# Optimization experiments

Hardware: AMD Instinct MI355X
Metric: run time of the kernel (lower is better)

## Reference

```python
import jax, jax.numpy as jnp
import numpy as np

B, S, E, H, FF = 4, 2048, 512, 8, 2048
DH = E // H
EPS = 1e-6


def setup_inputs() -> dict:
    key = jax.random.key(0)
    ks = jax.random.split(key, 16)
    sc = lambda fan_in: 1.0 / np.sqrt(fan_in)
    inp = {
        "x": jax.random.normal(ks[0], (B, S, E), dtype=jnp.float32),
        "src_mask": jnp.ones((B, 1, 1, S), dtype=jnp.int32),
        # attention projections, stored [in, out]
        "wq": jax.random.uniform(ks[1], (E, E), minval=-sc(E), maxval=sc(E)),
        "bq": jnp.zeros((E,), jnp.float32),
        "wk": jax.random.uniform(ks[2], (E, E), minval=-sc(E), maxval=sc(E)),
        "bk": jnp.zeros((E,), jnp.float32),
        "wv": jax.random.uniform(ks[3], (E, E), minval=-sc(E), maxval=sc(E)),
        "bv": jnp.zeros((E,), jnp.float32),
        "wo": jax.random.uniform(ks[4], (E, E), minval=-sc(E), maxval=sc(E)),
        "bo": jnp.zeros((E,), jnp.float32),
        # feed-forward
        "w1": jax.random.uniform(ks[5], (E, FF), minval=-sc(E), maxval=sc(E)),
        "b1": jnp.zeros((FF,), jnp.float32),
        "w2": jax.random.uniform(ks[6], (FF, E), minval=-sc(FF), maxval=sc(FF)),
        "b2": jnp.zeros((E,), jnp.float32),
        # addNormLayer scalar params (alpha init 1, bias init 0)
        "alpha1": jnp.ones((1,), jnp.float32),
        "beta1": jnp.zeros((1,), jnp.float32),
        "alpha2": jnp.ones((1,), jnp.float32),
        "beta2": jnp.zeros((1,), jnp.float32),
    }
    return inp


def _norm(x, alpha, beta):
    # matches torch: mean + unbiased std (ddof=1), eps added to std
    mean = jnp.mean(x, axis=-1, keepdims=True)
    std = jnp.std(x, axis=-1, keepdims=True, ddof=1)
    return alpha * (x - mean) / (std + EPS) + beta


def reference(x, src_mask, wq, bq, wk, bk, wv, bv, wo, bo,
              w1, b1, w2, b2, alpha1, beta1, alpha2, beta2):
    # --- residual 1: pre-norm self-attention ---
    n = _norm(x, alpha1, beta1)  # [B,S,E]
    q = (n @ wq + bq).reshape(B, S, H, DH).transpose(0, 2, 1, 3)  # [B,H,S,DH]
    k = (n @ wk + bk).reshape(B, S, H, DH).transpose(0, 2, 1, 3)
    v = (n @ wv + bv).reshape(B, S, H, DH).transpose(0, 2, 1, 3)
    scores = jnp.einsum('bhqd,bhkd->bhqk', q, k) / np.sqrt(DH)  # [B,H,S,S]
    scores = jnp.where(src_mask == 0, -1e9, scores)
    attn = jax.nn.softmax(scores, axis=-1)
    ctx = jnp.einsum('bhqk,bhkd->bhqd', attn, v)  # [B,H,S,DH]
    ctx = ctx.transpose(0, 2, 1, 3).reshape(B, S, E)
    x = x + (ctx @ wo + bo)
    # --- residual 2: pre-norm FFN ---
    n2 = _norm(x, alpha2, beta2)
    ff = jax.nn.relu(n2 @ w1 + b1) @ w2 + b2
    return x + ff
```

## Files before the change

### kernel.cpp

```cpp
#include <hip/hip_runtime.h>

typedef __bf16 bfrag __attribute__((ext_vector_type(8)));
typedef float f32x4 __attribute__((ext_vector_type(4)));
typedef unsigned short us8 __attribute__((ext_vector_type(8)));

__device__ __forceinline__ float bf2f(unsigned short s) {
  unsigned u = ((unsigned)s) << 16;
  float f;
  __builtin_memcpy(&f, &u, 4);
  return f;
}
__device__ __forceinline__ unsigned short f2bf(float f) {
  unsigned u;
  __builtin_memcpy(&u, &f, 4);
  u += 0x7fffu + ((u >> 16) & 1u);
  return (unsigned short)(u >> 16);
}
__device__ __forceinline__ float rdf(const void* p, size_t i, int isf) {
  return isf ? ((const float*)p)[i] : bf2f(((const unsigned short*)p)[i]);
}
__device__ __forceinline__ void gld16(const unsigned short* g, unsigned short* l) {
  __builtin_amdgcn_global_load_lds(
      (const __attribute__((address_space(1))) unsigned int*)g,
      (__attribute__((address_space(3))) unsigned int*)l, 16, 0, 0);
}

__global__ __launch_bounds__(256) void detect_k(
    const unsigned short* __restrict__ x, int* __restrict__ flag) {
  __shared__ int cnt;
  if (threadIdx.x == 0) cnt = 0;
  __syncthreads();
  int c = 0;
  for (int i = threadIdx.x; i < 4096; i += 256) {
    unsigned short s = x[2 * i];
    int e = (s >> 7) & 0xFF;
    if (e > 0xC2 || (e != 0 && e < 0x3D)) c++;
  }
  atomicAdd(&cnt, c);
  __syncthreads();
  if (threadIdx.x == 0) flag[0] = (cnt > 256) ? 1 : 0;
}

__global__ __launch_bounds__(256) void prep_k(
    const void* wq, const void* wk, const void* wv, const void* wo,
    const void* w1, const void* w2,
    unsigned short* wqT, unsigned short* wkT, unsigned short* wvT,
    unsigned short* woT, unsigned short* w1T, unsigned short* w2T,
    const void* bq, const void* bk, const void* bv, const void* bo,
    const void* b1, const void* b2, float* __restrict__ bcat,
    const int* __restrict__ flag) {
  __shared__ unsigned short tile[32][33];
  int isf = flag[0];
  int bid = blockIdx.x;
  int tid = threadIdx.x;
  if (bid >= 3072) {
    int i = (bid - 3072) * 256 + tid;
    if (i >= 4608) return;
    float v;
    if (i < 512) v = rdf(bq, i, isf);
    else if (i < 1024) v = rdf(bk, i - 512, isf);
    else if (i < 1536) v = rdf(bv, i - 1024, isf);
    else if (i < 2048) v = rdf(bo, i - 1536, isf);
    else if (i < 4096) v = rdf(b1, i - 2048, isf);
    else v = rdf(b2, i - 4096, isf);
    bcat[i] = v;
    return;
  }
  const void* W;
  unsigned short* Wt;
  int K, N, t;
  if (bid < 1024) {
    K = 512; N = 512; t = bid & 255;
    if (bid < 256) { W = wq; Wt = wqT; }
    else if (bid < 512) { W = wk; Wt = wkT; }
    else if (bid < 768) { W = wv; Wt = wvT; }
    else { W = wo; Wt = woT; }
  } else if (bid < 2048) {
    W = w1; Wt = w1T; K = 512; N = 2048; t = bid - 1024;
  } else {
    W = w2; Wt = w2T; K = 2048; N = 512; t = bid - 2048;
  }
  int nx = N >> 5;
  int n0 = (t % nx) * 32, k0 = (t / nx) * 32;
#pragma unroll
  for (int i = 0; i < 4; i++) {
    int e = tid + i * 256;
    int r = e >> 5, c = e & 31;
    tile[r][c] = f2bf(rdf(W, (size_t)(k0 + r) * N + n0 + c, isf));
  }
  __syncthreads();
#pragma unroll
  for (int i = 0; i < 4; i++) {
    int e = tid + i * 256;
    int r = e >> 5, c = e & 31;
    Wt[(size_t)(n0 + r) * K + k0 + c] = tile[c][r];
  }
}

__global__ __launch_bounds__(256) void vtrans_k(
    const unsigned short* __restrict__ qkb, unsigned short* __restrict__ vbt) {
  __shared__ unsigned short tile[32][33];
  int tid = threadIdx.x;
  int s0 = blockIdx.x * 32;
  int d0 = blockIdx.y * 32;
  int bh = blockIdx.z, b = bh >> 3, h = bh & 7;
#pragma unroll
  for (int i = 0; i < 4; i++) {
    int e = tid + i * 256;
    int r = e >> 5, c = e & 31;
    tile[r][c] = qkb[((size_t)b * 2048 + s0 + r) * 1536 + 1024 + h * 64 + d0 + c];
  }
  __syncthreads();
#pragma unroll
  for (int i = 0; i < 4; i++) {
    int e = tid + i * 256;
    int r = e >> 5, c = e & 31;
    vbt[((size_t)bh * 64 + d0 + r) * 2048 + s0 + c] = tile[c][r];
  }
}

template <int XMODE>
__global__ __launch_bounds__(256) void norm_k(
    const void* __restrict__ xin, const void* __restrict__ alpha,
    const void* __restrict__ beta, unsigned short* __restrict__ out,
    const int* __restrict__ flag) {
  constexpr int E = 512;
  int isf = flag[0];
  int xf = XMODE ? 1 : isf;
  int tid = threadIdx.x;
  int wave = tid >> 6, lane = tid & 63;
  size_t tok = (size_t)blockIdx.x * 4 + wave;
  float v[8];
  if (xf) {
    const float* xp = (const float*)xin + tok * E + lane * 8;
    float4 a0 = *(const float4*)xp;
    float4 a1 = *(const float4*)(xp + 4);
    v[0] = a0.x; v[1] = a0.y; v[2] = a0.z; v[3] = a0.w;
    v[4] = a1.x; v[5] = a1.y; v[6] = a1.z; v[7] = a1.w;
  } else {
    us8 u = *(const us8*)((const unsigned short*)xin + tok * E + lane * 8);
#pragma unroll
    for (int j = 0; j < 8; j++) v[j] = bf2f(u[j]);
  }
  float s = 0.f, sq = 0.f;
#pragma unroll
  for (int j = 0; j < 8; j++) { s += v[j]; sq += v[j] * v[j]; }
#pragma unroll
  for (int off = 1; off < 64; off <<= 1) {
    s += __shfl_xor(s, off, 64);
    sq += __shfl_xor(sq, off, 64);
  }
  float mean = s * (1.0f / 512.0f);
  float var = fmaxf((sq - 512.0f * mean * mean) * (1.0f / 511.0f), 0.0f);
  float inv = rdf(alpha, 0, isf) / (sqrtf(var) + 1e-6f);
  float be = rdf(beta, 0, isf);
  us8 ov;
#pragma unroll
  for (int j = 0; j < 8; j++) ov[j] = f2bf((v[j] - mean) * inv + be);
  *(us8*)((unsigned short*)out + tok * E + lane * 8) = ov;
}

template <int TN, int RES, int OUTM, int RELU>
__global__ __launch_bounds__(256) void gemm2_k(
    const unsigned short* __restrict__ A,
    const unsigned short* __restrict__ Bt,
    const float* __restrict__ bias,
    const void* __restrict__ res,
    void* __restrict__ outp,
    int N, int K, const int* __restrict__ flag) {
  constexpr int MT = (TN == 128) ? 4 : 2;
  __shared__ alignas(16) unsigned short As[128 * 32];
  __shared__ alignas(16) unsigned short Bs[TN * 32];
  int isf = flag[0];
  int outf32 = (OUTM == 1) || (OUTM == 2 && isf);
  int tid = threadIdx.x;
  int wave = tid >> 6, lane = tid & 63;
  int quad = lane >> 4, l16 = lane & 15;
  int wm = (TN == 128) ? (wave >> 1) : wave;
  int wn = (TN == 128) ? (wave & 1) : 0;
  size_t m0 = (size_t)blockIdx.x * 128;
  size_t n0 = (size_t)blockIdx.y * TN;

  int lrow = lane >> 2;
  int kseg = (lane & 3) * 8;

  const unsigned short* ag = A + (m0 + wave * 16 + lrow) * K + kseg;
  const unsigned short* bg = Bt + (n0 + wave * 16 + lrow) * K + kseg;
  unsigned short* asl = &As[(wave * 16) * 32];
  unsigned short* bsl = &Bs[(wave * 16) * 32];

  f32x4 acc[MT][4];
#pragma unroll
  for (int i = 0; i < MT; i++)
#pragma unroll
    for (int j = 0; j < 4; j++) acc[i][j] = {0.f, 0.f, 0.f, 0.f};

  for (int k0 = 0; k0 < K; k0 += 32) {
    __syncthreads();
    gld16(ag + k0, asl);
    gld16(ag + (size_t)64 * K + k0, asl + 64 * 32);
    gld16(bg + k0, bsl);
    if (TN == 128) gld16(bg + (size_t)64 * K + k0, bsl + 64 * 32);
    __syncthreads();
    bfrag af[MT], bf[4];
#pragma unroll
    for (int i = 0; i < MT; i++)
      af[i] = *(const bfrag*)&As[(wm * (MT * 16) + i * 16 + l16) * 32 + quad * 8];
#pragma unroll
    for (int j = 0; j < 4; j++)
      bf[j] = *(const bfrag*)&Bs[(wn * 64 + j * 16 + l16) * 32 + quad * 8];
#pragma unroll
    for (int i = 0; i < MT; i++)
#pragma unroll
      for (int j = 0; j < 4; j++)
        acc[i][j] = __builtin_amdgcn_mfma_f32_16x16x32_bf16(af[i], bf[j], acc[i][j], 0, 0, 0);
  }
#pragma unroll
  for (int j = 0; j < 4; j++) {
    size_t n = n0 + wn * 64 + j * 16 + l16;
    float bv = bias[n];
#pragma unroll
    for (int i = 0; i < MT; i++) {
#pragma unroll
      for (int r = 0; r < 4; r++) {
        size_t m = m0 + wm * (MT * 16) + i * 16 + quad * 4 + r;
        float vv = acc[i][j][r] + bv;
        if (RELU) vv = fmaxf(vv, 0.0f);
        if (RES == 1) vv += rdf(res, m * N + n, isf);
        else if (RES == 2) vv += ((const float*)res)[m * N + n];
        if (outf32) ((float*)outp)[m * N + n] = vv;
        else ((unsigned short*)outp)[m * N + n] = f2bf(vv);
      }
    }
  }
}

__global__ __launch_bounds__(256) void attn_k(
    const unsigned short* __restrict__ qkb,
    const unsigned short* __restrict__ vbt,
    const int* __restrict__ mask,
    unsigned short* __restrict__ ctx) {
  constexpr int S = 2048;
  __shared__ alignas(16) unsigned short Kt[64][72];
  __shared__ alignas(16) unsigned short Vt[64][72];
  __shared__ alignas(16) unsigned short Pl[4][16][68];
  __shared__ float mskf[64];
  int tid = threadIdx.x, wave = tid >> 6, lane = tid & 63;
  int quad = lane >> 4, l16 = lane & 15;
  int q0 = blockIdx.x * 64;
  int bh = blockIdx.y, b = bh >> 3, h = bh & 7;
  size_t rowbase = (size_t)b * S;

  bfrag qf0, qf1;
  {
    const unsigned short* qp =
        qkb + (rowbase + q0 + wave * 16 + l16) * 1536 + h * 64 + quad * 8;
    qf0 = *(const bfrag*)qp;
    qf1 = *(const bfrag*)(qp + 32);
  }
  f32x4 o[4] = {{0, 0, 0, 0}, {0, 0, 0, 0}, {0, 0, 0, 0}, {0, 0, 0, 0}};
  float l_i[4] = {0.f, 0.f, 0.f, 0.f};

  int srow = tid >> 2;
  int c0 = (tid & 3) * 8;
  const unsigned short* kbase = qkb + 512 + h * 64;
  const unsigned short* vrow = vbt + ((size_t)bh * 64 + srow) * S;
  const float SC = 0.18033688f;

  for (int kt = 0; kt < S; kt += 64) {
    __syncthreads();
    {
      const unsigned short* kp = kbase + (rowbase + kt + srow) * 1536;
      *(uint4*)&Kt[srow][c0]      = *(const uint4*)(kp + c0);
      *(uint4*)&Kt[srow][c0 + 32] = *(const uint4*)(kp + c0 + 32);
      *(uint4*)&Vt[srow][c0]      = *(const uint4*)(vrow + kt + c0);
      *(uint4*)&Vt[srow][c0 + 32] = *(const uint4*)(vrow + kt + c0 + 32);
    }
    if (tid < 64) mskf[tid] = mask[rowbase + kt + tid] ? 0.0f : -1e5f;
    __syncthreads();

    float pr[4][4];
#pragma unroll
    for (int nt = 0; nt < 4; nt++) {
      f32x4 s = {0, 0, 0, 0};
      bfrag k0f = *(const bfrag*)&Kt[nt * 16 + l16][quad * 8];
      bfrag k1f = *(const bfrag*)&Kt[nt * 16 + l16][32 + quad * 8];
      s = __builtin_amdgcn_mfma_f32_16x16x32_bf16(qf0, k0f, s, 0, 0, 0);
      s = __builtin_amdgcn_mfma_f32_16x16x32_bf16(qf1, k1f, s, 0, 0, 0);
      float mb = mskf[nt * 16 + l16];
#pragma unroll
      for (int r = 0; r < 4; r++) {
        float p = __builtin_amdgcn_exp2f(fminf(fmaf(s[r], SC, mb), 50.0f));
        pr[nt][r] = p;
        unsigned u;
        __builtin_memcpy(&u, &p, 4);
        Pl[wave][quad * 4 + r][nt * 16 + l16] = (unsigned short)(u >> 16);
      }
    }
#pragma unroll
    for (int r = 0; r < 4; r++)
      l_i[r] += (pr[0][r] + pr[1][r]) + (pr[2][r] + pr[3][r]);
    bfrag pa0 = *(const bfrag*)&Pl[wave][l16][quad * 8];
    bfrag pa1 = *(const bfrag*)&Pl[wave][l16][32 + quad * 8];
#pragma unroll
    for (int dt = 0; dt < 4; dt++) {
      bfrag v0 = *(const bfrag*)&Vt[dt * 16 + l16][quad * 8];
      bfrag v1 = *(const bfrag*)&Vt[dt * 16 + l16][32 + quad * 8];
      o[dt] = __builtin_amdgcn_mfma_f32_16x16x32_bf16(pa0, v0, o[dt], 0, 0, 0);
      o[dt] = __builtin_amdgcn_mfma_f32_16x16x32_bf16(pa1, v1, o[dt], 0, 0, 0);
    }
  }
#pragma unroll
  for (int r = 0; r < 4; r++) {
#pragma unroll
    for (int off = 1; off < 16; off <<= 1) l_i[r] += __shfl_xor(l_i[r], off, 64);
    l_i[r] = 1.0f / fmaxf(l_i[r], 1e-30f);
  }
#pragma unroll
  for (int dt = 0; dt < 4; dt++) {
#pragma unroll
    for (int r = 0; r < 4; r++) {
      size_t qrow = rowbase + q0 + wave * 16 + quad * 4 + r;
      ctx[qrow * 512 + h * 64 + dt * 16 + l16] = f2bf(o[dt][r] * l_i[r]);
    }
  }
}

extern "C" void kernel_launch(void* const* d_in, const int* in_sizes, int n_in,
                              void* d_out, int out_size, void* d_ws, size_t ws_size,
                              hipStream_t stream) {
  const unsigned short* x = (const unsigned short*)d_in[0];
  const int* mask         = (const int*)d_in[1];
  const void* wq = d_in[2];  const void* bq = d_in[3];
  const void* wk = d_in[4];  const void* bk = d_in[5];
  const void* wv = d_in[6];  const void* bv = d_in[7];
  const void* wo = d_in[8];  const void* bo = d_in[9];
  const void* w1 = d_in[10]; const void* b1 = d_in[11];
  const void* w2 = d_in[12]; const void* b2 = d_in[13];
  const void* alpha1 = d_in[14]; const void* beta1 = d_in[15];
  const void* alpha2 = d_in[16]; const void* beta2 = d_in[17];

  char* ws = (char*)d_ws;
  int* flag            = (int*)(ws + 0);
  unsigned short* wqkvT= (unsigned short*)(ws + 65536);
  unsigned short* wqT  = wqkvT;
  unsigned short* wkT  = (unsigned short*)(ws + 589824);
  unsigned short* wvT  = (unsigned short*)(ws + 1114112);
  unsigned short* woT  = (unsigned short*)(ws + 1638400);
  unsigned short* w1T  = (unsigned short*)(ws + 2162688);
  unsigned short* w2T  = (unsigned short*)(ws + 4259840);
  float*          bcat = (float*)         (ws + 6356992);
  float*          x1   = (float*)         (ws + 6422528);
  unsigned short* n1   = (unsigned short*)(ws + 23199744);
  unsigned short* ctx  = n1;
  unsigned short* n2   = n1;
  unsigned short* qkb  = (unsigned short*)(ws + 31588352);
  unsigned short* vbt  = (unsigned short*)(ws + 56754176);
  unsigned short* ff1  = qkb;

  dim3 blk(256);

  detect_k<<<1, blk, 0, stream>>>(x, flag);
  prep_k<<<3090, blk, 0, stream>>>(wq, wk, wv, wo, w1, w2,
                                   wqT, wkT, wvT, woT, w1T, w2T,
                                   bq, bk, bv, bo, b1, b2, bcat, flag);

  norm_k<0><<<2048, blk, 0, stream>>>(x, alpha1, beta1, n1, flag);
  gemm2_k<128, 0, 0, 0><<<dim3(64, 12), blk, 0, stream>>>(n1, wqkvT, bcat, nullptr, qkb, 1536, 512, flag);
  vtrans_k<<<dim3(64, 2, 32), blk, 0, stream>>>(qkb, vbt);
  attn_k<<<dim3(32, 32), blk, 0, stream>>>(qkb, vbt, mask, ctx);
  gemm2_k<64, 1, 1, 0><<<dim3(64, 8), blk, 0, stream>>>(ctx, woT, bcat + 1536, (const void*)x, x1, 512, 512, flag);
  norm_k<1><<<2048, blk, 0, stream>>>(x1, alpha2, beta2, n2, flag);
  gemm2_k<128, 0, 0, 1><<<dim3(64, 16), blk, 0, stream>>>(n2, w1T, bcat + 2048, nullptr, ff1, 2048, 512, flag);
  gemm2_k<64, 2, 2, 0><<<dim3(64, 8), blk, 0, stream>>>(ff1, w2T, bcat + 4096, x1, d_out, 512, 2048, flag);
}
```

Baseline: 324.5 us.

## Merge setup kernels and process two query tiles per attention block

```diff
diff --git a/kernel.cpp b/kernel.cpp
--- a/kernel.cpp
+++ b/kernel.cpp
@@ -25,111 +25,14 @@
       (__attribute__((address_space(3))) unsigned int*)l, 16, 0, 0);
 }
 
-__global__ __launch_bounds__(256) void detect_k(
-    const unsigned short* __restrict__ x, int* __restrict__ flag) {
-  __shared__ int cnt;
-  if (threadIdx.x == 0) cnt = 0;
-  __syncthreads();
-  int c = 0;
-  for (int i = threadIdx.x; i < 4096; i += 256) {
-    unsigned short s = x[2 * i];
-    int e = (s >> 7) & 0xFF;
-    if (e > 0xC2 || (e != 0 && e < 0x3D)) c++;
-  }
-  atomicAdd(&cnt, c);
-  __syncthreads();
-  if (threadIdx.x == 0) flag[0] = (cnt > 256) ? 1 : 0;
-}
-
-__global__ __launch_bounds__(256) void prep_k(
-    const void* wq, const void* wk, const void* wv, const void* wo,
-    const void* w1, const void* w2,
-    unsigned short* wqT, unsigned short* wkT, unsigned short* wvT,
-    unsigned short* woT, unsigned short* w1T, unsigned short* w2T,
-    const void* bq, const void* bk, const void* bv, const void* bo,
-    const void* b1, const void* b2, float* __restrict__ bcat,
-    const int* __restrict__ flag) {
-  __shared__ unsigned short tile[32][33];
-  int isf = flag[0];
-  int bid = blockIdx.x;
-  int tid = threadIdx.x;
-  if (bid >= 3072) {
-    int i = (bid - 3072) * 256 + tid;
-    if (i >= 4608) return;
-    float v;
-    if (i < 512) v = rdf(bq, i, isf);
-    else if (i < 1024) v = rdf(bk, i - 512, isf);
-    else if (i < 1536) v = rdf(bv, i - 1024, isf);
-    else if (i < 2048) v = rdf(bo, i - 1536, isf);
-    else if (i < 4096) v = rdf(b1, i - 2048, isf);
-    else v = rdf(b2, i - 4096, isf);
-    bcat[i] = v;
-    return;
-  }
-  const void* W;
-  unsigned short* Wt;
-  int K, N, t;
-  if (bid < 1024) {
-    K = 512; N = 512; t = bid & 255;
-    if (bid < 256) { W = wq; Wt = wqT; }
-    else if (bid < 512) { W = wk; Wt = wkT; }
-    else if (bid < 768) { W = wv; Wt = wvT; }
-    else { W = wo; Wt = woT; }
-  } else if (bid < 2048) {
-    W = w1; Wt = w1T; K = 512; N = 2048; t = bid - 1024;
-  } else {
-    W = w2; Wt = w2T; K = 2048; N = 512; t = bid - 2048;
-  }
-  int nx = N >> 5;
-  int n0 = (t % nx) * 32, k0 = (t / nx) * 32;
-#pragma unroll
-  for (int i = 0; i < 4; i++) {
-    int e = tid + i * 256;
-    int r = e >> 5, c = e & 31;
-    tile[r][c] = f2bf(rdf(W, (size_t)(k0 + r) * N + n0 + c, isf));
-  }
-  __syncthreads();
-#pragma unroll
-  for (int i = 0; i < 4; i++) {
-    int e = tid + i * 256;
-    int r = e >> 5, c = e & 31;
-    Wt[(size_t)(n0 + r) * K + k0 + c] = tile[c][r];
-  }
-}
-
-__global__ __launch_bounds__(256) void vtrans_k(
-    const unsigned short* __restrict__ qkb, unsigned short* __restrict__ vbt) {
-  __shared__ unsigned short tile[32][33];
-  int tid = threadIdx.x;
-  int s0 = blockIdx.x * 32;
-  int d0 = blockIdx.y * 32;
-  int bh = blockIdx.z, b = bh >> 3, h = bh & 7;
-#pragma unroll
-  for (int i = 0; i < 4; i++) {
-    int e = tid + i * 256;
-    int r = e >> 5, c = e & 31;
-    tile[r][c] = qkb[((size_t)b * 2048 + s0 + r) * 1536 + 1024 + h * 64 + d0 + c];
-  }
-  __syncthreads();
-#pragma unroll
-  for (int i = 0; i < 4; i++) {
-    int e = tid + i * 256;
-    int r = e >> 5, c = e & 31;
-    vbt[((size_t)bh * 64 + d0 + r) * 2048 + s0 + c] = tile[c][r];
-  }
-}
-
 template <int XMODE>
-__global__ __launch_bounds__(256) void norm_k(
-    const void* __restrict__ xin, const void* __restrict__ alpha,
-    const void* __restrict__ beta, unsigned short* __restrict__ out,
-    const int* __restrict__ flag) {
+__device__ void norm_unit(const void* xin, const void* alpha, const void* beta,
+                          unsigned short* out, int isf, int u) {
   constexpr int E = 512;
-  int isf = flag[0];
   int xf = XMODE ? 1 : isf;
   int tid = threadIdx.x;
   int wave = tid >> 6, lane = tid & 63;
-  size_t tok = (size_t)blockIdx.x * 4 + wave;
+  size_t tok = (size_t)u * 4 + wave;
   float v[8];
   if (xf) {
     const float* xp = (const float*)xin + tok * E + lane * 8;
@@ -138,9 +41,9 @@
     v[0] = a0.x; v[1] = a0.y; v[2] = a0.z; v[3] = a0.w;
     v[4] = a1.x; v[5] = a1.y; v[6] = a1.z; v[7] = a1.w;
   } else {
-    us8 u = *(const us8*)((const unsigned short*)xin + tok * E + lane * 8);
-#pragma unroll
-    for (int j = 0; j < 8; j++) v[j] = bf2f(u[j]);
+    us8 uu = *(const us8*)((const unsigned short*)xin + tok * E + lane * 8);
+#pragma unroll
+    for (int j = 0; j < 8; j++) v[j] = bf2f(uu[j]);
   }
   float s = 0.f, sq = 0.f;
 #pragma unroll
@@ -157,7 +60,115 @@
   us8 ov;
 #pragma unroll
   for (int j = 0; j < 8; j++) ov[j] = f2bf((v[j] - mean) * inv + be);
-  *(us8*)((unsigned short*)out + tok * E + lane * 8) = ov;
+  *(us8*)(out + tok * E + lane * 8) = ov;
+}
+
+__global__ __launch_bounds__(256) void setup_k(
+    const unsigned short* __restrict__ x16,
+    const void* wq, const void* wk, const void* wv, const void* wo,
+    const void* w1, const void* w2,
+    unsigned short* wqkvT, unsigned short* woT,
+    unsigned short* w1T, unsigned short* w2T,
+    const void* bq, const void* bk, const void* bv, const void* bo,
+    const void* b1, const void* b2, float* __restrict__ bcat,
+    const void* alpha1, const void* beta1, unsigned short* __restrict__ n1,
+    int* __restrict__ flag) {
+  __shared__ unsigned short tile[32][33];
+  __shared__ int s_cnt;
+  int tid = threadIdx.x;
+  int bid = blockIdx.x;
+  if (tid == 0) s_cnt = 0;
+  __syncthreads();
+  {
+    int c = 0;
+    for (int i = tid; i < 4096; i += 256) {
+      unsigned short s = x16[2 * i];
+      int e = (s >> 7) & 0xFF;
+      if (e > 0xC2 || (e != 0 && e < 0x3D)) c++;
+    }
+    atomicAdd(&s_cnt, c);
+  }
+  __syncthreads();
+  const int isf = (s_cnt > 256) ? 1 : 0;
+  if (bid == 0 && tid == 0) flag[0] = isf;
+
+  if (bid >= 3090) {
+    norm_unit<0>(x16, alpha1, beta1, n1, isf, bid - 3090);
+    return;
+  }
+  if (bid >= 3072) {
+    int i = (bid - 3072) * 256 + tid;
+    if (i < 4608) {
+      float v;
+      if (i < 512) v = rdf(bq, i, isf);
+      else if (i < 1024) v = rdf(bk, i - 512, isf);
+      else if (i < 1536) v = rdf(bv, i - 1024, isf);
+      else if (i < 2048) v = rdf(bo, i - 1536, isf);
+      else if (i < 4096) v = rdf(b1, i - 2048, isf);
+      else v = rdf(b2, i - 4096, isf);
+      bcat[i] = v;
+    }
+    return;
+  }
+  const void* W;
+  unsigned short* Wt;
+  int K, N, t;
+  if (bid < 1024) {
+    K = 512; N = 512; t = bid & 255;
+    if (bid < 256) { W = wq; Wt = wqkvT; }
+    else if (bid < 512) { W = wk; Wt = wqkvT + 262144; }
+    else if (bid < 768) { W = wv; Wt = wqkvT + 524288; }
+    else { W = wo; Wt = woT; }
+  } else if (bid < 2048) {
+    W = w1; Wt = w1T; K = 512; N = 2048; t = bid - 1024;
+  } else {
+    W = w2; Wt = w2T; K = 2048; N = 512; t = bid - 2048;
+  }
+  int nx = N >> 5;
+  int n0 = (t % nx) * 32, k0 = (t / nx) * 32;
+#pragma unroll
+  for (int i = 0; i < 4; i++) {
+    int e = tid + i * 256;
+    int r = e >> 5, c = e & 31;
+    tile[r][c] = f2bf(rdf(W, (size_t)(k0 + r) * N + n0 + c, isf));
+  }
+  __syncthreads();
+#pragma unroll
+  for (int i = 0; i < 4; i++) {
+    int e = tid + i * 256;
+    int r = e >> 5, c = e & 31;
+    Wt[(size_t)(n0 + r) * K + k0 + c] = tile[c][r];
+  }
+}
+
+__global__ __launch_bounds__(256) void vtrans_k(
+    const unsigned short* __restrict__ qkb, unsigned short* __restrict__ vbt) {
+  __shared__ unsigned short tile[32][33];
+  int tid = threadIdx.x;
+  int u = blockIdx.x;
+  int s0 = (u & 63) * 32;
+  int d0 = ((u >> 6) & 1) * 32;
+  int bh = u >> 7, b = bh >> 3, h = bh & 7;
+#pragma unroll
+  for (int i = 0; i < 4; i++) {
+    int e = tid + i * 256;
+    int r = e >> 5, c = e & 31;
+    tile[r][c] = qkb[((size_t)b * 2048 + s0 + r) * 1536 + 1024 + h * 64 + d0 + c];
+  }
+  __syncthreads();
+#pragma unroll
+  for (int i = 0; i < 4; i++) {
+    int e = tid + i * 256;
+    int r = e >> 5, c = e & 31;
+    vbt[((size_t)bh * 64 + d0 + r) * 2048 + s0 + c] = tile[c][r];
+  }
+}
+
+__global__ __launch_bounds__(256) void norm2_k(
+    const void* __restrict__ xin, const void* __restrict__ alpha,
+    const void* __restrict__ beta, unsigned short* __restrict__ out,
+    const int* __restrict__ flag) {
+  norm_unit<1>(xin, alpha, beta, out, flag[0], blockIdx.x);
 }
 
 template <int TN, int RES, int OUTM, int RELU>
@@ -241,25 +252,31 @@
     const int* __restrict__ mask,
     unsigned short* __restrict__ ctx) {
   constexpr int S = 2048;
-  __shared__ alignas(16) unsigned short Kt[64][72];
-  __shared__ alignas(16) unsigned short Vt[64][72];
-  __shared__ alignas(16) unsigned short Pl[4][16][68];
+  __shared__ alignas(16) unsigned short Kt[64][70];
+  __shared__ alignas(16) unsigned short Vt[64][70];
+  __shared__ alignas(16) unsigned short Pl[4][16][70];
   __shared__ float mskf[64];
   int tid = threadIdx.x, wave = tid >> 6, lane = tid & 63;
   int quad = lane >> 4, l16 = lane & 15;
-  int q0 = blockIdx.x * 64;
-  int bh = blockIdx.y, b = bh >> 3, h = bh & 7;
+  int q0 = (blockIdx.x & 15) * 128;
+  int bh = blockIdx.x >> 4, b = bh >> 3, h = bh & 7;
   size_t rowbase = (size_t)b * S;
-
-  bfrag qf0, qf1;
-  {
+  unsigned short* PlW = &Pl[wave][0][0];
+
+  bfrag qf[2][2];
+#pragma unroll
+  for (int mi = 0; mi < 2; mi++) {
     const unsigned short* qp =
-        qkb + (rowbase + q0 + wave * 16 + l16) * 1536 + h * 64 + quad * 8;
-    qf0 = *(const bfrag*)qp;
-    qf1 = *(const bfrag*)(qp + 32);
-  }
-  f32x4 o[4] = {{0, 0, 0, 0}, {0, 0, 0, 0}, {0, 0, 0, 0}, {0, 0, 0, 0}};
-  float l_i[4] = {0.f, 0.f, 0.f, 0.f};
+        qkb + (rowbase + q0 + mi * 64 + wave * 16 + l16) * 1536 + h * 64 + quad * 8;
+    qf[mi][0] = *(const bfrag*)qp;
+    qf[mi][1] = *(const bfrag*)(qp + 32);
+  }
+  f32x4 o[2][4];
+  float l_i[2][4];
+#pragma unroll
+  for (int mi = 0; mi < 2; mi++)
+#pragma unroll
+    for (int j = 0; j < 4; j++) { o[mi][j] = {0.f, 0.f, 0.f, 0.f}; l_i[mi][j] = 0.f; }
 
   int srow = tid >> 2;
   int c0 = (tid & 3) * 8;
@@ -279,49 +296,56 @@
     if (tid < 64) mskf[tid] = mask[rowbase + kt + tid] ? 0.0f : -1e5f;
     __syncthreads();
 
-    float pr[4][4];
-#pragma unroll
-    for (int nt = 0; nt < 4; nt++) {
-      f32x4 s = {0, 0, 0, 0};
-      bfrag k0f = *(const bfrag*)&Kt[nt * 16 + l16][quad * 8];
-      bfrag k1f = *(const bfrag*)&Kt[nt * 16 + l16][32 + quad * 8];
-      s = __builtin_amdgcn_mfma_f32_16x16x32_bf16(qf0, k0f, s, 0, 0, 0);
-      s = __builtin_amdgcn_mfma_f32_16x16x32_bf16(qf1, k1f, s, 0, 0, 0);
-      float mb = mskf[nt * 16 + l16];
+#pragma unroll
+    for (int mi = 0; mi < 2; mi++) {
+      float pr[4][4];
+#pragma unroll
+      for (int nt = 0; nt < 4; nt++) {
+        f32x4 s = {0, 0, 0, 0};
+        bfrag k0f = *(const bfrag*)&Kt[nt * 16 + l16][quad * 8];
+        bfrag k1f = *(const bfrag*)&Kt[nt * 16 + l16][32 + quad * 8];
+        s = __builtin_amdgcn_mfma_f32_16x16x32_bf16(qf[mi][0], k0f, s, 0, 0, 0);
+        s = __builtin_amdgcn_mfma_f32_16x16x32_bf16(qf[mi][1], k1f, s, 0, 0, 0);
+        float mb = mskf[nt * 16 + l16];
+#pragma unroll
+        for (int r = 0; r < 4; r++) {
+          float p = __builtin_amdgcn_exp2f(fminf(fmaf(s[r], SC, mb), 50.0f));
+          pr[nt][r] = p;
+          unsigned u;
+          __builtin_memcpy(&u, &p, 4);
+          PlW[(quad * 4 + r) * 70 + nt * 16 + l16] = (unsigned short)(u >> 16);
+        }
+      }
+#pragma unroll
+      for (int r = 0; r < 4; r++)
+        l_i[mi][r] += (pr[0][r] + pr[1][r]) + (pr[2][r] + pr[3][r]);
+      bfrag pa0 = *(const bfrag*)&PlW[l16 * 70 + quad * 8];
+      bfrag pa1 = *(const bfrag*)&PlW[l16 * 70 + 32 + quad * 8];
+#pragma unroll
+      for (int dt = 0; dt < 4; dt++) {
+        bfrag v0 = *(const bfrag*)&Vt[dt * 16 + l16][quad * 8];
+        bfrag v1 = *(const bfrag*)&Vt[dt * 16 + l16][32 + quad * 8];
+        o[mi][dt] = __builtin_amdgcn_mfma_f32_16x16x32_bf16(pa0, v0, o[mi][dt], 0, 0, 0);
+        o[mi][dt] = __builtin_amdgcn_mfma_f32_16x16x32_bf16(pa1, v1, o[mi][dt], 0, 0, 0);
+      }
+    }
+  }
+#pragma unroll
+  for (int mi = 0; mi < 2; mi++) {
+#pragma unroll
+    for (int r = 0; r < 4; r++) {
+#pragma unroll
+      for (int off = 1; off < 16; off <<= 1)
+        l_i[mi][r] += __shfl_xor(l_i[mi][r], off, 64);
+      l_i[mi][r] = 1.0f / fmaxf(l_i[mi][r], 1e-30f);
+    }
+#pragma unroll
+    for (int dt = 0; dt < 4; dt++) {
 #pragma unroll
       for (int r = 0; r < 4; r++) {
-        float p = __builtin_amdgcn_exp2f(fminf(fmaf(s[r], SC, mb), 50.0f));
-        pr[nt][r] = p;
-        unsigned u;
-        __builtin_memcpy(&u, &p, 4);
-        Pl[wave][quad * 4 + r][nt * 16 + l16] = (unsigned short)(u >> 16);
+        size_t qrow = rowbase + q0 + mi * 64 + wave * 16 + quad * 4 + r;
+        ctx[qrow * 512 + h * 64 + dt * 16 + l16] = f2bf(o[mi][dt][r] * l_i[mi][r]);
       }
-    }
-#pragma unroll
-    for (int r = 0; r < 4; r++)
-      l_i[r] += (pr[0][r] + pr[1][r]) + (pr[2][r] + pr[3][r]);
-    bfrag pa0 = *(const bfrag*)&Pl[wave][l16][quad * 8];
-    bfrag pa1 = *(const bfrag*)&Pl[wave][l16][32 + quad * 8];
-#pragma unroll
-    for (int dt = 0; dt < 4; dt++) {
-      bfrag v0 = *(const bfrag*)&Vt[dt * 16 + l16][quad * 8];
-      bfrag v1 = *(const bfrag*)&Vt[dt * 16 + l16][32 + quad * 8];
-      o[dt] = __builtin_amdgcn_mfma_f32_16x16x32_bf16(pa0, v0, o[dt], 0, 0, 0);
-      o[dt] = __builtin_amdgcn_mfma_f32_16x16x32_bf16(pa1, v1, o[dt], 0, 0, 0);
-    }
-  }
-#pragma unroll
-  for (int r = 0; r < 4; r++) {
-#pragma unroll
-    for (int off = 1; off < 16; off <<= 1) l_i[r] += __shfl_xor(l_i[r], off, 64);
-    l_i[r] = 1.0f / fmaxf(l_i[r], 1e-30f);
-  }
-#pragma unroll
-  for (int dt = 0; dt < 4; dt++) {
-#pragma unroll
-    for (int r = 0; r < 4; r++) {
-      size_t qrow = rowbase + q0 + wave * 16 + quad * 4 + r;
-      ctx[qrow * 512 + h * 64 + dt * 16 + l16] = f2bf(o[dt][r] * l_i[r]);
     }
   }
 }
@@ -343,34 +367,27 @@
   char* ws = (char*)d_ws;
   int* flag            = (int*)(ws + 0);
   unsigned short* wqkvT= (unsigned short*)(ws + 65536);
-  unsigned short* wqT  = wqkvT;
-  unsigned short* wkT  = (unsigned short*)(ws + 589824);
-  unsigned short* wvT  = (unsigned short*)(ws + 1114112);
   unsigned short* woT  = (unsigned short*)(ws + 1638400);
   unsigned short* w1T  = (unsigned short*)(ws + 2162688);
   unsigned short* w2T  = (unsigned short*)(ws + 4259840);
   float*          bcat = (float*)         (ws + 6356992);
   float*          x1   = (float*)         (ws + 6422528);
   unsigned short* n1   = (unsigned short*)(ws + 23199744);
-  unsigned short* ctx  = n1;
-  unsigned short* n2   = n1;
   unsigned short* qkb  = (unsigned short*)(ws + 31588352);
   unsigned short* vbt  = (unsigned short*)(ws + 56754176);
   unsigned short* ff1  = qkb;
 
   dim3 blk(256);
 
-  detect_k<<<1, blk, 0, stream>>>(x, flag);
-  prep_k<<<3090, blk, 0, stream>>>(wq, wk, wv, wo, w1, w2,
-                                   wqT, wkT, wvT, woT, w1T, w2T,
-                                   bq, bk, bv, bo, b1, b2, bcat, flag);
-
-  norm_k<0><<<2048, blk, 0, stream>>>(x, alpha1, beta1, n1, flag);
+  setup_k<<<5138, blk, 0, stream>>>(x, wq, wk, wv, wo, w1, w2,
+                                    wqkvT, woT, w1T, w2T,
+                                    bq, bk, bv, bo, b1, b2, bcat,
+                                    alpha1, beta1, n1, flag);
   gemm2_k<128, 0, 0, 0><<<dim3(64, 12), blk, 0, stream>>>(n1, wqkvT, bcat, nullptr, qkb, 1536, 512, flag);
-  vtrans_k<<<dim3(64, 2, 32), blk, 0, stream>>>(qkb, vbt);
-  attn_k<<<dim3(32, 32), blk, 0, stream>>>(qkb, vbt, mask, ctx);
-  gemm2_k<64, 1, 1, 0><<<dim3(64, 8), blk, 0, stream>>>(ctx, woT, bcat + 1536, (const void*)x, x1, 512, 512, flag);
-  norm_k<1><<<2048, blk, 0, stream>>>(x1, alpha2, beta2, n2, flag);
-  gemm2_k<128, 0, 0, 1><<<dim3(64, 16), blk, 0, stream>>>(n2, w1T, bcat + 2048, nullptr, ff1, 2048, 512, flag);
+  vtrans_k<<<4096, blk, 0, stream>>>(qkb, vbt);
+  attn_k<<<512, blk, 0, stream>>>(qkb, vbt, mask, n1);
+  gemm2_k<64, 1, 1, 0><<<dim3(64, 8), blk, 0, stream>>>(n1, woT, bcat + 1536, (const void*)x, x1, 512, 512, flag);
+  norm2_k<<<2048, blk, 0, stream>>>(x1, alpha2, beta2, n1, flag);
+  gemm2_k<128, 0, 0, 1><<<dim3(64, 16), blk, 0, stream>>>(n1, w1T, bcat + 2048, nullptr, ff1, 2048, 512, flag);
   gemm2_k<64, 2, 2, 0><<<dim3(64, 8), blk, 0, stream>>>(ff1, w2T, bcat + 4096, x1, d_out, 512, 2048, flag);
 }
```

New measurement: 375.7 us. 1.16x slower.

## Fuse all stages into one persistent kernel with software grid barriers

Applied to the files above, without the earlier changes.

```diff
diff --git a/kernel.cpp b/kernel.cpp
--- a/kernel.cpp
+++ b/kernel.cpp
@@ -25,63 +25,51 @@
       (__attribute__((address_space(3))) unsigned int*)l, 16, 0, 0);
 }
 
-__global__ __launch_bounds__(256) void detect_k(
-    const unsigned short* __restrict__ x, int* __restrict__ flag) {
-  __shared__ int cnt;
-  if (threadIdx.x == 0) cnt = 0;
-  __syncthreads();
-  int c = 0;
-  for (int i = threadIdx.x; i < 4096; i += 256) {
-    unsigned short s = x[2 * i];
-    int e = (s >> 7) & 0xFF;
-    if (e > 0xC2 || (e != 0 && e < 0x3D)) c++;
-  }
-  atomicAdd(&cnt, c);
-  __syncthreads();
-  if (threadIdx.x == 0) flag[0] = (cnt > 256) ? 1 : 0;
-}
-
-__global__ __launch_bounds__(256) void prep_k(
-    const void* wq, const void* wk, const void* wv, const void* wo,
-    const void* w1, const void* w2,
-    unsigned short* wqT, unsigned short* wkT, unsigned short* wvT,
-    unsigned short* woT, unsigned short* w1T, unsigned short* w2T,
-    const void* bq, const void* bk, const void* bv, const void* bo,
-    const void* b1, const void* b2, float* __restrict__ bcat,
-    const int* __restrict__ flag) {
-  __shared__ unsigned short tile[32][33];
-  int isf = flag[0];
-  int bid = blockIdx.x;
+struct MArgs {
+  const unsigned short* x16;
+  const int* mask;
+  const void *wq, *wk, *wv, *wo, *w1, *w2;
+  const void *bq, *bk, *bv, *bo, *b1, *b2;
+  const void *alpha1, *beta1, *alpha2, *beta2;
+  void* d_out;
+  unsigned* bar;
+  unsigned* gen;
+  unsigned short* wqkvT;
+  unsigned short* woT;
+  unsigned short* w1T;
+  unsigned short* w2T;
+  float* bcat;
+  float* x1;
+  unsigned short* n1;
+  unsigned short* qkb;
+  unsigned short* vbt;
+};
+
+__device__ __forceinline__ void gbar(unsigned* bar, unsigned* gen, unsigned nb) {
+  __syncthreads();
+  if (threadIdx.x == 0) {
+    __threadfence();
+    unsigned g = __hip_atomic_load(gen, __ATOMIC_RELAXED, __HIP_MEMORY_SCOPE_AGENT);
+    if (atomicAdd(bar, 1u) == nb - 1u) {
+      __hip_atomic_store(bar, 0u, __ATOMIC_RELAXED, __HIP_MEMORY_SCOPE_AGENT);
+      __threadfence();
+      atomicAdd(gen, 1u);
+    } else {
+      while (__hip_atomic_load(gen, __ATOMIC_RELAXED, __HIP_MEMORY_SCOPE_AGENT) == g)
+        __builtin_amdgcn_s_sleep(8);
+      __threadfence();
+    }
+  }
+  __syncthreads();
+}
+
+__device__ void trans_unit(const void* W, unsigned short* Wt, int K, int N,
+                           int t, int isf, char* SM) {
+  auto tile = (unsigned short(*)[33])SM;
   int tid = threadIdx.x;
-  if (bid >= 3072) {
-    int i = (bid - 3072) * 256 + tid;
-    if (i >= 4608) return;
-    float v;
-    if (i < 512) v = rdf(bq, i, isf);
-    else if (i < 1024) v = rdf(bk, i - 512, isf);
-    else if (i < 1536) v = rdf(bv, i - 1024, isf);
-    else if (i < 2048) v = rdf(bo, i - 1536, isf);
-    else if (i < 4096) v = rdf(b1, i - 2048, isf);
-    else v = rdf(b2, i - 4096, isf);
-    bcat[i] = v;
-    return;
-  }
-  const void* W;
-  unsigned short* Wt;
-  int K, N, t;
-  if (bid < 1024) {
-    K = 512; N = 512; t = bid & 255;
-    if (bid < 256) { W = wq; Wt = wqT; }
-    else if (bid < 512) { W = wk; Wt = wkT; }
-    else if (bid < 768) { W = wv; Wt = wvT; }
-    else { W = wo; Wt = woT; }
-  } else if (bid < 2048) {
-    W = w1; Wt = w1T; K = 512; N = 2048; t = bid - 1024;
-  } else {
-    W = w2; Wt = w2T; K = 2048; N = 512; t = bid - 2048;
-  }
   int nx = N >> 5;
   int n0 = (t % nx) * 32, k0 = (t / nx) * 32;
+  __syncthreads();
 #pragma unroll
   for (int i = 0; i < 4; i++) {
     int e = tid + i * 256;
@@ -97,13 +85,14 @@
   }
 }
 
-__global__ __launch_bounds__(256) void vtrans_k(
-    const unsigned short* __restrict__ qkb, unsigned short* __restrict__ vbt) {
-  __shared__ unsigned short tile[32][33];
+__device__ void vtrans_unit(const unsigned short* qkb, unsigned short* vbt,
+                            int u, char* SM) {
+  auto tile = (unsigned short(*)[33])SM;
   int tid = threadIdx.x;
-  int s0 = blockIdx.x * 32;
-  int d0 = blockIdx.y * 32;
-  int bh = blockIdx.z, b = bh >> 3, h = bh & 7;
+  int s0 = (u & 63) * 32;
+  int d0 = ((u >> 6) & 1) * 32;
+  int bh = u >> 7, b = bh >> 3, h = bh & 7;
+  __syncthreads();
 #pragma unroll
   for (int i = 0; i < 4; i++) {
     int e = tid + i * 256;
@@ -120,16 +109,13 @@
 }
 
 template <int XMODE>
-__global__ __launch_bounds__(256) void norm_k(
-    const void* __restrict__ xin, const void* __restrict__ alpha,
-    const void* __restrict__ beta, unsigned short* __restrict__ out,
-    const int* __restrict__ flag) {
+__device__ void norm_unit(const void* xin, const void* alpha, const void* beta,
+                          unsigned short* out, int isf, int u) {
   constexpr int E = 512;
-  int isf = flag[0];
   int xf = XMODE ? 1 : isf;
   int tid = threadIdx.x;
   int wave = tid >> 6, lane = tid & 63;
-  size_t tok = (size_t)blockIdx.x * 4 + wave;
+  size_t tok = (size_t)u * 4 + wave;
   float v[8];
   if (xf) {
     const float* xp = (const float*)xin + tok * E + lane * 8;
@@ -138,9 +124,9 @@
     v[0] = a0.x; v[1] = a0.y; v[2] = a0.z; v[3] = a0.w;
     v[4] = a1.x; v[5] = a1.y; v[6] = a1.z; v[7] = a1.w;
   } else {
-    us8 u = *(const us8*)((const unsigned short*)xin + tok * E + lane * 8);
-#pragma unroll
-    for (int j = 0; j < 8; j++) v[j] = bf2f(u[j]);
+    us8 uu = *(const us8*)((const unsigned short*)xin + tok * E + lane * 8);
+#pragma unroll
+    for (int j = 0; j < 8; j++) v[j] = bf2f(uu[j]);
   }
   float s = 0.f, sq = 0.f;
 #pragma unroll
@@ -157,29 +143,26 @@
   us8 ov;
 #pragma unroll
   for (int j = 0; j < 8; j++) ov[j] = f2bf((v[j] - mean) * inv + be);
-  *(us8*)((unsigned short*)out + tok * E + lane * 8) = ov;
+  *(us8*)(out + tok * E + lane * 8) = ov;
 }
 
 template <int TN, int RES, int OUTM, int RELU>
-__global__ __launch_bounds__(256) void gemm2_k(
-    const unsigned short* __restrict__ A,
-    const unsigned short* __restrict__ Bt,
-    const float* __restrict__ bias,
-    const void* __restrict__ res,
-    void* __restrict__ outp,
-    int N, int K, const int* __restrict__ flag) {
+__device__ void gemm_tile(const unsigned short* __restrict__ A,
+                          const unsigned short* __restrict__ Bt,
+                          const float* __restrict__ bias,
+                          const void* __restrict__ res, void* __restrict__ outp,
+                          int N, int K, int isf, int mi, int ni, char* SM) {
   constexpr int MT = (TN == 128) ? 4 : 2;
-  __shared__ alignas(16) unsigned short As[128 * 32];
-  __shared__ alignas(16) unsigned short Bs[TN * 32];
-  int isf = flag[0];
+  unsigned short* As = (unsigned short*)SM;
+  unsigned short* Bs = (unsigned short*)(SM + 8192);
   int outf32 = (OUTM == 1) || (OUTM == 2 && isf);
   int tid = threadIdx.x;
   int wave = tid >> 6, lane = tid & 63;
   int quad = lane >> 4, l16 = lane & 15;
   int wm = (TN == 128) ? (wave >> 1) : wave;
   int wn = (TN == 128) ? (wave & 1) : 0;
-  size_t m0 = (size_t)blockIdx.x * 128;
-  size_t n0 = (size_t)blockIdx.y * TN;
+  size_t m0 = (size_t)mi * 128;
+  size_t n0 = (size_t)ni * TN;
 
   int lrow = lane >> 2;
   int kseg = (lane & 3) * 8;
@@ -235,20 +218,19 @@
   }
 }
 
-__global__ __launch_bounds__(256) void attn_k(
-    const unsigned short* __restrict__ qkb,
-    const unsigned short* __restrict__ vbt,
-    const int* __restrict__ mask,
-    unsigned short* __restrict__ ctx) {
+__device__ void attn_tile(const unsigned short* __restrict__ qkb,
+                          const unsigned short* __restrict__ vbt,
+                          const int* __restrict__ mask,
+                          unsigned short* __restrict__ ctx,
+                          int q0, int bh, char* SM) {
   constexpr int S = 2048;
-  __shared__ alignas(16) unsigned short Kt[64][72];
-  __shared__ alignas(16) unsigned short Vt[64][72];
-  __shared__ alignas(16) unsigned short Pl[4][16][68];
-  __shared__ float mskf[64];
+  auto Kt = (unsigned short(*)[72])(SM);
+  auto Vt = (unsigned short(*)[72])(SM + 9216);
+  float* mskf = (float*)(SM + 27136);
   int tid = threadIdx.x, wave = tid >> 6, lane = tid & 63;
   int quad = lane >> 4, l16 = lane & 15;
-  int q0 = blockIdx.x * 64;
-  int bh = blockIdx.y, b = bh >> 3, h = bh & 7;
+  unsigned short* PlW = (unsigned short*)(SM + 18432) + wave * 16 * 68;
+  int b = bh >> 3, h = bh & 7;
   size_t rowbase = (size_t)b * S;
 
   bfrag qf0, qf1;
@@ -294,14 +276,14 @@
         pr[nt][r] = p;
         unsigned u;
         __builtin_memcpy(&u, &p, 4);
-        Pl[wave][quad * 4 + r][nt * 16 + l16] = (unsigned short)(u >> 16);
+        PlW[(quad * 4 + r) * 68 + nt * 16 + l16] = (unsigned short)(u >> 16);
       }
     }
 #pragma unroll
     for (int r = 0; r < 4; r++)
       l_i[r] += (pr[0][r] + pr[1][r]) + (pr[2][r] + pr[3][r]);
-    bfrag pa0 = *(const bfrag*)&Pl[wave][l16][quad * 8];
-    bfrag pa1 = *(const bfrag*)&Pl[wave][l16][32 + quad * 8];
+    bfrag pa0 = *(const bfrag*)&PlW[l16 * 68 + quad * 8];
+    bfrag pa1 = *(const bfrag*)&PlW[l16 * 68 + 32 + quad * 8];
 #pragma unroll
     for (int dt = 0; dt < 4; dt++) {
       bfrag v0 = *(const bfrag*)&Vt[dt * 16 + l16][quad * 8];
@@ -326,51 +308,102 @@
   }
 }
 
+__global__ __launch_bounds__(256, 2) void mega_k(MArgs a) {
+  __shared__ alignas(16) char SM[28672];
+  __shared__ int s_cnt;
+  int tid = threadIdx.x;
+  int bid = blockIdx.x;
+
+  if (tid == 0) s_cnt = 0;
+  __syncthreads();
+  {
+    int c = 0;
+    for (int i = tid; i < 4096; i += 256) {
+      unsigned short s = a.x16[2 * i];
+      int e = (s >> 7) & 0xFF;
+      if (e > 0xC2 || (e != 0 && e < 0x3D)) c++;
+    }
+    atomicAdd(&s_cnt, c);
+  }
+  __syncthreads();
+  const int isf = (s_cnt > 256) ? 1 : 0;
+
+  for (int u = bid; u < 5138; u += 512) {
+    if (u < 3072) {
+      if (u < 256)       trans_unit(a.wq, a.wqkvT,          512, 512, u, isf, SM);
+      else if (u < 512)  trans_unit(a.wk, a.wqkvT + 262144, 512, 512, u - 256, isf, SM);
+      else if (u < 768)  trans_unit(a.wv, a.wqkvT + 524288, 512, 512, u - 512, isf, SM);
+      else if (u < 1024) trans_unit(a.wo, a.woT,            512, 512, u - 768, isf, SM);
+      else if (u < 2048) trans_unit(a.w1, a.w1T,  512, 2048, u - 1024, isf, SM);
+      else               trans_unit(a.w2, a.w2T, 2048,  512, u - 2048, isf, SM);
+    } else if (u < 3090) {
+      int i = (u - 3072) * 256 + tid;
+      if (i < 4608) {
+        float v;
+        if (i < 512) v = rdf(a.bq, i, isf);
+        else if (i < 1024) v = rdf(a.bk, i - 512, isf);
+        else if (i < 1536) v = rdf(a.bv, i - 1024, isf);
+        else if (i < 2048) v = rdf(a.bo, i - 1536, isf);
+        else if (i < 4096) v = rdf(a.b1, i - 2048, isf);
+        else v = rdf(a.b2, i - 4096, isf);
+        a.bcat[i] = v;
+      }
+    } else {
+      norm_unit<0>(a.x16, a.alpha1, a.beta1, a.n1, isf, u - 3090);
+    }
+  }
+  gbar(a.bar, a.gen, 512);
+  for (int t = bid; t < 768; t += 512)
+    gemm_tile<128, 0, 0, 0>(a.n1, a.wqkvT, a.bcat, nullptr, a.qkb,
+                            1536, 512, isf, t & 63, t >> 6, SM);
+  gbar(a.bar, a.gen, 512);
+  for (int u = bid; u < 4096; u += 512) vtrans_unit(a.qkb, a.vbt, u, SM);
+  gbar(a.bar, a.gen, 512);
+  for (int t = bid; t < 1024; t += 512)
+    attn_tile(a.qkb, a.vbt, a.mask, a.n1, (t & 31) * 64, t >> 5, SM);
+  gbar(a.bar, a.gen, 512);
+  gemm_tile<64, 1, 1, 0>(a.n1, a.woT, a.bcat + 1536, (const void*)a.x16, a.x1,
+                         512, 512, isf, bid & 63, bid >> 6, SM);
+  gbar(a.bar, a.gen, 512);
+  for (int u = bid; u < 2048; u += 512)
+    norm_unit<1>(a.x1, a.alpha2, a.beta2, a.n1, isf, u);
+  gbar(a.bar, a.gen, 512);
+  for (int t = bid; t < 1024; t += 512)
+    gemm_tile<128, 0, 0, 1>(a.n1, a.w1T, a.bcat + 2048, nullptr, a.qkb,
+                            2048, 512, isf, t & 63, t >> 6, SM);
+  gbar(a.bar, a.gen, 512);
+  gemm_tile<64, 2, 2, 0>(a.qkb, a.w2T, a.bcat + 4096, a.x1, a.d_out,
+                         512, 2048, isf, bid & 63, bid >> 6, SM);
+}
+
 extern "C" void kernel_launch(void* const* d_in, const int* in_sizes, int n_in,
                               void* d_out, int out_size, void* d_ws, size_t ws_size,
                               hipStream_t stream) {
-  const unsigned short* x = (const unsigned short*)d_in[0];
-  const int* mask         = (const int*)d_in[1];
-  const void* wq = d_in[2];  const void* bq = d_in[3];
-  const void* wk = d_in[4];  const void* bk = d_in[5];
-  const void* wv = d_in[6];  const void* bv = d_in[7];
-  const void* wo = d_in[8];  const void* bo = d_in[9];
-  const void* w1 = d_in[10]; const void* b1 = d_in[11];
-  const void* w2 = d_in[12]; const void* b2 = d_in[13];
-  const void* alpha1 = d_in[14]; const void* beta1 = d_in[15];
-  const void* alpha2 = d_in[16]; const void* beta2 = d_in[17];
-
   char* ws = (char*)d_ws;
-  int* flag            = (int*)(ws + 0);
-  unsigned short* wqkvT= (unsigned short*)(ws + 65536);
-  unsigned short* wqT  = wqkvT;
-  unsigned short* wkT  = (unsigned short*)(ws + 589824);
-  unsigned short* wvT  = (unsigned short*)(ws + 1114112);
-  unsigned short* woT  = (unsigned short*)(ws + 1638400);
-  unsigned short* w1T  = (unsigned short*)(ws + 2162688);
-  unsigned short* w2T  = (unsigned short*)(ws + 4259840);
-  float*          bcat = (float*)         (ws + 6356992);
-  float*          x1   = (float*)         (ws + 6422528);
-  unsigned short* n1   = (unsigned short*)(ws + 23199744);
-  unsigned short* ctx  = n1;
-  unsigned short* n2   = n1;
-  unsigned short* qkb  = (unsigned short*)(ws + 31588352);
-  unsigned short* vbt  = (unsigned short*)(ws + 56754176);
-  unsigned short* ff1  = qkb;
-
-  dim3 blk(256);
-
-  detect_k<<<1, blk, 0, stream>>>(x, flag);
-  prep_k<<<3090, blk, 0, stream>>>(wq, wk, wv, wo, w1, w2,
-                                   wqT, wkT, wvT, woT, w1T, w2T,
-                                   bq, bk, bv, bo, b1, b2, bcat, flag);
-
-  norm_k<0><<<2048, blk, 0, stream>>>(x, alpha1, beta1, n1, flag);
-  gemm2_k<128, 0, 0, 0><<<dim3(64, 12), blk, 0, stream>>>(n1, wqkvT, bcat, nullptr, qkb, 1536, 512, flag);
-  vtrans_k<<<dim3(64, 2, 32), blk, 0, stream>>>(qkb, vbt);
-  attn_k<<<dim3(32, 32), blk, 0, stream>>>(qkb, vbt, mask, ctx);
-  gemm2_k<64, 1, 1, 0><<<dim3(64, 8), blk, 0, stream>>>(ctx, woT, bcat + 1536, (const void*)x, x1, 512, 512, flag);
-  norm_k<1><<<2048, blk, 0, stream>>>(x1, alpha2, beta2, n2, flag);
-  gemm2_k<128, 0, 0, 1><<<dim3(64, 16), blk, 0, stream>>>(n2, w1T, bcat + 2048, nullptr, ff1, 2048, 512, flag);
-  gemm2_k<64, 2, 2, 0><<<dim3(64, 8), blk, 0, stream>>>(ff1, w2T, bcat + 4096, x1, d_out, 512, 2048, flag);
-}
+  MArgs a;
+  a.x16 = (const unsigned short*)d_in[0];
+  a.mask = (const int*)d_in[1];
+  a.wq = d_in[2];  a.bq = d_in[3];
+  a.wk = d_in[4];  a.bk = d_in[5];
+  a.wv = d_in[6];  a.bv = d_in[7];
+  a.wo = d_in[8];  a.bo = d_in[9];
+  a.w1 = d_in[10]; a.b1 = d_in[11];
+  a.w2 = d_in[12]; a.b2 = d_in[13];
+  a.alpha1 = d_in[14]; a.beta1 = d_in[15];
+  a.alpha2 = d_in[16]; a.beta2 = d_in[17];
+  a.d_out = d_out;
+  a.bar   = (unsigned*)(ws + 0);
+  a.gen   = (unsigned*)(ws + 128);
+  a.wqkvT = (unsigned short*)(ws + 65536);
+  a.woT   = (unsigned short*)(ws + 1638400);
+  a.w1T   = (unsigned short*)(ws + 2162688);
+  a.w2T   = (unsigned short*)(ws + 4259840);
+  a.bcat  = (float*)         (ws + 6356992);
+  a.x1    = (float*)         (ws + 6422528);
+  a.n1    = (unsigned short*)(ws + 23199744);
+  a.qkb   = (unsigned short*)(ws + 31588352);
+  a.vbt   = (unsigned short*)(ws + 56754176);
+
+  hipMemsetAsync(ws, 0, 256, stream);
+  mega_k<<<512, 256, 0, stream>>>(a);
+}
```

After: 528.9 us. 1.63x slower.
